# Performance work log

Hardware: AMD Instinct MI355X
Metric: run time of the kernel (lower is better)

Reference implementation:

```python
import jax, jax.numpy as jnp
import numpy as np

HIDDEN = 100   # units per head
HEADS = 8
LAYERS = 3
ALPHA = 0.2    # tf.nn.leaky_relu default


def setup_inputs() -> dict:
    key = jax.random.key(0)
    ks = jax.random.split(key, 10)
    n, feat, E = 50000, 32, 800000
    d = HIDDEN * HEADS  # 800
    scale = 0.05
    node_states = jax.random.normal(ks[0], (n, feat), jnp.float32)
    # TF code's repeat/bincount segment-softmax assumes edges sorted by source
    src = jnp.sort(jax.random.randint(ks[1], (E,), 0, n, dtype=jnp.int32))
    dst = jax.random.randint(ks[2], (E,), 0, n, dtype=jnp.int32)
    W_pre = jax.random.normal(ks[3], (feat, d), jnp.float32) * scale
    b_pre = jnp.zeros((d,), jnp.float32)
    kernels = jax.random.normal(ks[4], (LAYERS, HEADS, d, HIDDEN), jnp.float32) * scale
    att = jax.random.normal(ks[5], (LAYERS, HEADS, 2 * HIDDEN, 1), jnp.float32) * scale
    Wl = jax.random.normal(ks[6], (d, 1), jnp.float32) * scale
    bl = jnp.zeros((1,), jnp.float32)
    Wc = jax.random.normal(ks[7], (n, 1), jnp.float32) * scale
    bc = jnp.zeros((1,), jnp.float32)
    return dict(node_states=node_states, src=src, dst=dst, W_pre=W_pre, b_pre=b_pre,
                kernels=kernels, att=att, Wl=Wl, bl=bl, Wc=Wc, bc=bc)


def _gat_head(x, src, dst, K, A, n):
    # x: (n, d); K: (d, u); A: (2u,) attention vector
    Ht = x @ K                          # (n, u)
    # concat([Ht[src], Ht[dst]]) @ A == Ht[src]@A[:u] + Ht[dst]@A[u:]
    s = Ht @ A[:HIDDEN]                 # (n,)
    t = Ht @ A[HIDDEN:]                 # (n,)
    e = jax.nn.leaky_relu(s[src] + t[dst], ALPHA)   # (E,)
    w = jnp.exp(jnp.clip(e, -2.0, 2.0))             # (E,)
    denom = jax.ops.segment_sum(w, src, num_segments=n)  # (n,)
    wn = w / denom[src]                              # segment softmax, (E,)
    # weighted scatter-add of neighbor features
    return jax.ops.segment_sum(Ht[dst] * wn[:, None], src, num_segments=n)  # (n, u)


def reference(node_states, src, dst, W_pre, b_pre, kernels, att, Wl, bl, Wc, bc):
    n = node_states.shape[0]
    x = jax.nn.relu(node_states @ W_pre + b_pre)     # (n, 800)
    for l in range(LAYERS):
        heads = [_gat_head(x, src, dst, kernels[l, h], att[l, h, :, 0], n)
                 for h in range(HEADS)]
        x = jax.nn.relu(jnp.concatenate(heads, axis=-1)) + x  # residual
    logits = jnp.squeeze(x @ Wl + bl, -1)            # (n,)
    return logits @ Wc + bc                          # critic value, (1,)
```

## Files before the change

### kernel.cpp

```cpp
#include <hip/hip_runtime.h>
#include <math.h>

#define HIDDEN 100
#define HEADS 8
#define D 800
#define ALPHA 0.2f

typedef unsigned short ushort;
typedef unsigned int uint;
typedef __attribute__((ext_vector_type(8))) short bf16x8;
typedef __attribute__((ext_vector_type(4))) float f32x4;

__device__ inline float bf2f(ushort u) { uint x = ((uint)u) << 16; return __uint_as_float(x); }
__device__ inline ushort f2bf(float f) {
    uint u = __float_as_uint(f);
    u += 0x7FFF + ((u >> 16) & 1);
    return (ushort)(u >> 16);
}

__device__ inline void gl_lds16(const void* g, void* l) {
    __builtin_amdgcn_global_load_lds((const __attribute__((address_space(1))) void*)g,
                                     (__attribute__((address_space(3))) void*)l, 16, 0, 0);
}

__global__ void k_rowptr(const int* __restrict__ src, int E, int n, int* __restrict__ row_ptr) {
    int i = blockIdx.x * blockDim.x + threadIdx.x;
    if (i > n) return;
    int lo = 0, hi = E;
    while (lo < hi) { int mid = (lo + hi) >> 1; if (src[mid] < i) lo = mid + 1; else hi = mid; }
    row_ptr[i] = lo;
}

__global__ void k_repack(const float* __restrict__ kin, ushort* __restrict__ bsp) {
    int gid = blockIdx.x * blockDim.x + threadIdx.x;
    if (gid >= 3 * D * D) return;
    int l = gid / (D * D);
    int rem = gid % (D * D);
    int nn = rem / D;
    int k = rem % D;
    int h = nn / HIDDEN, c = nn % HIDDEN;
    float v = kin[((size_t)(l * HEADS + h) * D + k) * HIDDEN + c];
    bsp[((size_t)l * D + nn) * D + k] = f2bf(v);
}

__global__ __launch_bounds__(256) void k_pre(const float* __restrict__ ns, const float* __restrict__ W,
                                             const float* __restrict__ b, ushort* __restrict__ xh,
                                             ushort* __restrict__ xl, int n) {
    int j = blockIdx.x * 256 + threadIdx.x;
    if (j >= D) return;
    float wk[32];
#pragma unroll
    for (int k = 0; k < 32; k++) wk[k] = W[k * D + j];
    float bj = b[j];
    int r0 = blockIdx.y * 32;
    int r1 = min(r0 + 32, n);
    for (int r = r0; r < r1; r++) {
        float acc = bj;
#pragma unroll
        for (int k = 0; k < 32; k++) acc += ns[r * 32 + k] * wk[k];
        acc = fmaxf(acc, 0.f);
        ushort h = f2bf(acc);
        xh[(size_t)r * D + j] = h;
        xl[(size_t)r * D + j] = f2bf(acc - bf2f(h));
    }
}

__global__ __launch_bounds__(256) void k_gemm(const ushort* __restrict__ xh, const ushort* __restrict__ xl,
                                              const ushort* __restrict__ Bsp, ushort* __restrict__ C, int M) {
    __shared__ __align__(16) ushort Af[2][16 * 512];
    __shared__ __align__(16) ushort Bf[2][10 * 512];

    int d = blockIdx.x;
    int q = d & 7, m = d >> 3;
    int c = m % 5, j = m / 5;
    int r = j * 8 + q;
    int nrb = (M + 127) >> 7;
    if (r >= nrb) return;
    int row0 = r * 128, col0 = c * 160;

    int t = threadIdx.x;
    int w = t >> 6, lane = t & 63;
    int wr = w >> 1, wc = w & 1;
    int l15 = lane & 15, ks = lane >> 4;

    const ushort* srcA[4];
    int ldsA[4];
#pragma unroll
    for (int i = 0; i < 4; i++) {
        int g = i * 4 + w;
        int mat = g >> 3, tile = g & 7;
        int row = min(row0 + tile * 16 + l15, M - 1);
        srcA[i] = (mat ? xl : xh) + (size_t)row * D + ks * 8;
        ldsA[i] = g * 512;
    }
    int bcnt = (w < 2) ? 2 : 3;
    int bbase = (w < 2) ? 2 * w : 4 + 3 * (w - 2);
    const ushort* srcB[3];
    int ldsB[3];
#pragma unroll
    for (int i = 0; i < 3; i++) {
        int tile = bbase + i;
        if (tile > 9) tile = 9;
        int col = col0 + tile * 16 + l15;
        srcB[i] = Bsp + (size_t)col * D + ks * 8;
        ldsB[i] = tile * 512;
    }

    f32x4 acc[4][5] = {};

    auto stage = [&](int buf, int k0) {
#pragma unroll
        for (int i = 0; i < 4; i++) gl_lds16(srcA[i] + k0, &Af[buf][ldsA[i]]);
        for (int i = 0; i < bcnt; i++) gl_lds16(srcB[i] + k0, &Bf[buf][ldsB[i]]);
    };
    auto compute = [&](int buf) {
        bf16x8 bh[5];
#pragma unroll
        for (int ni = 0; ni < 5; ni++)
            bh[ni] = *(const bf16x8*)&Bf[buf][(wc * 5 + ni) * 512 + lane * 8];
#pragma unroll
        for (int mi = 0; mi < 4; mi++) {
            int tA = wr * 4 + mi;
            bf16x8 ah = *(const bf16x8*)&Af[buf][tA * 512 + lane * 8];
            bf16x8 al = *(const bf16x8*)&Af[buf][(8 + tA) * 512 + lane * 8];
#pragma unroll
            for (int ni = 0; ni < 5; ni++) {
                acc[mi][ni] = __builtin_amdgcn_mfma_f32_16x16x32_bf16(ah, bh[ni], acc[mi][ni], 0, 0, 0);
                acc[mi][ni] = __builtin_amdgcn_mfma_f32_16x16x32_bf16(al, bh[ni], acc[mi][ni], 0, 0, 0);
            }
        }
    };

    stage(0, 0);
    for (int kt = 0; kt < 25; kt++) {
        if (kt < 24) {
            stage((kt + 1) & 1, (kt + 1) * 32);
            if (w < 2) asm volatile("s_waitcnt vmcnt(6)" ::: "memory");
            else       asm volatile("s_waitcnt vmcnt(7)" ::: "memory");
        } else {
            asm volatile("s_waitcnt vmcnt(0)" ::: "memory");
        }
        __builtin_amdgcn_s_barrier();
        compute(kt & 1);
        __builtin_amdgcn_s_barrier();
    }

#pragma unroll
    for (int mi = 0; mi < 4; mi++) {
#pragma unroll
        for (int ni = 0; ni < 5; ni++) {
            int gr0 = row0 + wr * 64 + mi * 16 + ks * 4;
            int gc = col0 + wc * 80 + ni * 16 + l15;
#pragma unroll
            for (int rr = 0; rr < 4; rr++) {
                int gr = gr0 + rr;
                if (gr < M) C[(size_t)gr * D + gc] = f2bf(acc[mi][ni][rr]);
            }
        }
    }
}

__global__ __launch_bounds__(256) void k_st(const ushort* __restrict__ Ht, const float* __restrict__ att_l,
                                            float* __restrict__ s_all, float* __restrict__ t_all, int n) {
    int gid = blockIdx.x * blockDim.x + threadIdx.x;
    if (gid >= n * HEADS) return;
    int i = gid >> 3, h = gid & 7;
    const uint2* hp2 = (const uint2*)(Ht + (size_t)i * D + h * HIDDEN);
    const float* As = att_l + h * 2 * HIDDEN;
    const float* At = As + HIDDEN;
    float s = 0.f, t = 0.f;
#pragma unroll 5
    for (int q = 0; q < 25; q++) {
        uint2 v = hp2[q];
        float f0 = bf2f((ushort)(v.x & 0xFFFF)), f1 = bf2f((ushort)(v.x >> 16));
        float f2 = bf2f((ushort)(v.y & 0xFFFF)), f3 = bf2f((ushort)(v.y >> 16));
        int c = q * 4;
        s += f0 * As[c] + f1 * As[c + 1] + f2 * As[c + 2] + f3 * As[c + 3];
        t += f0 * At[c] + f1 * At[c + 1] + f2 * At[c + 2] + f3 * At[c + 3];
    }
    s_all[gid] = s;
    t_all[gid] = t;
}

__global__ __launch_bounds__(256) void k_edge(const ushort* __restrict__ Ht, ushort* __restrict__ xh,
                                              ushort* __restrict__ xl,
                                              const float* __restrict__ s_all, const float* __restrict__ t_all,
                                              const int* __restrict__ dst, const int* __restrict__ row_ptr,
                                              int n) {
    int i = blockIdx.x;
    int t = threadIdx.x;
    __shared__ float lw[32][8];
    __shared__ int ld[32];
    int e0 = row_ptr[i], e1 = row_ptr[i + 1];
    int h = t / 25;
    int el = t >> 3, hh = t & 7;
    float s_ih = s_all[i * 8 + hh];
    float acc0 = 0, acc1 = 0, acc2 = 0, acc3 = 0, den = 0;

    for (int base = e0; base < e1; base += 32) {
        int cnt = min(32, e1 - base);
        __syncthreads();
        if (el < cnt) {
            int dd = dst[base + el];
            float ev = s_ih + t_all[dd * 8 + hh];
            ev = ev >= 0.f ? ev : ALPHA * ev;
            ev = fminf(fmaxf(ev, -2.f), 2.f);
            lw[el][hh] = __expf(ev);
            if (hh == 0) ld[el] = dd;
        }
        __syncthreads();
        if (t < 200) {
#pragma unroll 4
            for (int e = 0; e < cnt; e++) {
                int dd = ld[e];
                uint2 v = *(const uint2*)(Ht + (size_t)dd * D + t * 4);
                float wgt = lw[e][h];
                acc0 += wgt * bf2f((ushort)(v.x & 0xFFFF));
                acc1 += wgt * bf2f((ushort)(v.x >> 16));
                acc2 += wgt * bf2f((ushort)(v.y & 0xFFFF));
                acc3 += wgt * bf2f((ushort)(v.y >> 16));
                den += wgt;
            }
        }
    }
    if (t < 200) {
        size_t off = (size_t)i * D + t * 4;
        uint2 vh = *(uint2*)(xh + off);
        uint2 vl = *(uint2*)(xl + off);
        float x0 = bf2f((ushort)(vh.x & 0xFFFF)) + bf2f((ushort)(vl.x & 0xFFFF));
        float x1 = bf2f((ushort)(vh.x >> 16))    + bf2f((ushort)(vl.x >> 16));
        float x2 = bf2f((ushort)(vh.y & 0xFFFF)) + bf2f((ushort)(vl.y & 0xFFFF));
        float x3 = bf2f((ushort)(vh.y >> 16))    + bf2f((ushort)(vl.y >> 16));
        float inv = den > 0.f ? 1.f / den : 0.f;
        x0 += fmaxf(acc0 * inv, 0.f);
        x1 += fmaxf(acc1 * inv, 0.f);
        x2 += fmaxf(acc2 * inv, 0.f);
        x3 += fmaxf(acc3 * inv, 0.f);
        ushort h0 = f2bf(x0), h1 = f2bf(x1), h2 = f2bf(x2), h3 = f2bf(x3);
        ushort l0 = f2bf(x0 - bf2f(h0)), l1 = f2bf(x1 - bf2f(h1));
        ushort l2 = f2bf(x2 - bf2f(h2)), l3 = f2bf(x3 - bf2f(h3));
        *(uint2*)(xh + off) = make_uint2((uint)h0 | ((uint)h1 << 16), (uint)h2 | ((uint)h3 << 16));
        *(uint2*)(xl + off) = make_uint2((uint)l0 | ((uint)l1 << 16), (uint)l2 | ((uint)l3 << 16));
    }
}

__global__ __launch_bounds__(256) void k_final(const ushort* __restrict__ xh, const ushort* __restrict__ xl,
                                               const float* __restrict__ Wl, const float* __restrict__ bl,
                                               const float* __restrict__ Wc, float* __restrict__ fpart, int n) {
    __shared__ float part[4];
    int lane = threadIdx.x & 63, w = threadIdx.x >> 6;
    int wid = blockIdx.x * 4 + w;
    int nw = gridDim.x * 4;
    float p = 0.f;
    for (int i = wid; i < n; i += nw) {
        float dot = 0.f;
#pragma unroll
        for (int r = 0; r < 13; r++) {
            int j = r * 64 + lane;
            if (j < D) {
                size_t off = (size_t)i * D + j;
                dot += (bf2f(xh[off]) + bf2f(xl[off])) * Wl[j];
            }
        }
#pragma unroll
        for (int off = 32; off; off >>= 1) dot += __shfl_xor(dot, off);
        if (lane == 0) p += (dot + bl[0]) * Wc[i];
    }
    if (lane == 0) part[w] = p;
    __syncthreads();
    if (threadIdx.x == 0) fpart[blockIdx.x] = part[0] + part[1] + part[2] + part[3];
}

__global__ __launch_bounds__(64) void k_reduce(const float* __restrict__ fpart, const float* __restrict__ bc,
                                               float* __restrict__ out, int nb) {
    if (threadIdx.x == 0) {
        float s = 0.f;
        for (int q = 0; q < nb; q++) s += fpart[q];
        out[0] = s + bc[0];
    }
}

__global__ void k_sentinel(float* out) { out[0] = 12345.0f; }

extern "C" void kernel_launch(void* const* d_in, const int* in_sizes, int n_in,
                              void* d_out, int out_size, void* d_ws, size_t ws_size,
                              hipStream_t stream) {
    const float* ns   = (const float*)d_in[0];
    const int*   src  = (const int*)d_in[1];
    const int*   dst  = (const int*)d_in[2];
    const float* Wpre = (const float*)d_in[3];
    const float* bpre = (const float*)d_in[4];
    const float* kern = (const float*)d_in[5];
    const float* att  = (const float*)d_in[6];
    const float* Wl   = (const float*)d_in[7];
    const float* bl   = (const float*)d_in[8];
    const float* Wc   = (const float*)d_in[9];
    const float* bc   = (const float*)d_in[10];
    int n = in_sizes[9];
    int E = in_sizes[1];

    size_t need = 0;
    auto sz = [&](size_t bytes) { size_t o = need; need += (bytes + 255) & ~255ull; return o; };
    size_t o_xh    = sz((size_t)n * D * 2);
    size_t o_xl    = sz((size_t)n * D * 2);
    size_t o_Ht    = sz((size_t)n * D * 2);
    size_t o_bsp   = sz(3ull * D * D * 2);
    size_t o_s     = sz((size_t)n * 8 * 4);
    size_t o_t     = sz((size_t)n * 8 * 4);
    size_t o_rp    = sz(((size_t)n + 1) * 4);
    size_t o_fp    = sz(128 * 4);

    if (need > ws_size) {
        k_sentinel<<<1, 1, 0, stream>>>((float*)d_out);
        return;
    }

    char* ws = (char*)d_ws;
    ushort* xh    = (ushort*)(ws + o_xh);
    ushort* xl    = (ushort*)(ws + o_xl);
    ushort* Ht    = (ushort*)(ws + o_Ht);
    ushort* bsp   = (ushort*)(ws + o_bsp);
    float*  s_all = (float*)(ws + o_s);
    float*  t_all = (float*)(ws + o_t);
    int*    row_ptr = (int*)(ws + o_rp);
    float*  fpart = (float*)(ws + o_fp);

    k_rowptr<<<(n + 1 + 255) / 256, 256, 0, stream>>>(src, E, n, row_ptr);
    k_repack<<<(3 * D * D + 255) / 256, 256, 0, stream>>>(kern, bsp);
    dim3 gpre((D + 255) / 256, (n + 31) / 32);
    k_pre<<<gpre, 256, 0, stream>>>(ns, Wpre, bpre, xh, xl, n);

    int nrb = (n + 127) / 128;
    int grid_g = 8 * (((nrb + 7) / 8) * 5);
    for (int l = 0; l < 3; l++) {
        k_gemm<<<grid_g, 256, 0, stream>>>(xh, xl, bsp + (size_t)l * D * D, Ht, n);
        k_st<<<(n * HEADS + 255) / 256, 256, 0, stream>>>(Ht, att + l * HEADS * 2 * HIDDEN, s_all, t_all, n);
        k_edge<<<n, 256, 0, stream>>>(Ht, xh, xl, s_all, t_all, dst, row_ptr, n);
    }

    k_final<<<120, 256, 0, stream>>>(xh, xl, Wl, bl, Wc, fpart, n);
    k_reduce<<<1, 64, 0, stream>>>(fpart, bc, (float*)d_out, 120);
}
```

Measured before the change: 1.432 ms.

## Store Ht head-major and process one head per block in edge gather

The GEMM epilogue now writes Ht in head-major layout [head][node][100], and s/t scores are stored head-major too. The edge kernel now assigns each block one head and 10 source nodes, 25 threads per node. Each thread walks its node's edges directly and recomputes the attention weight itself, with no shared-memory staging or barriers. The aim is to keep each head's 10 MB slice of Ht hot in L2 while gathering, and to drop synchronisation. In exchange, dst and t are read redundantly, 6 of 256 threads sit idle, and GEMM stores become strided.

Measured after the change: 1.575 ms. 1.1x slower.

```diff
diff --git a/kernel.cpp b/kernel.cpp
--- a/kernel.cpp
+++ b/kernel.cpp
@@ -146,15 +146,17 @@
     }
 
 #pragma unroll
-    for (int mi = 0; mi < 4; mi++) {
-#pragma unroll
-        for (int ni = 0; ni < 5; ni++) {
+    for (int ni = 0; ni < 5; ni++) {
+        int gc = col0 + wc * 80 + ni * 16 + l15;
+        int hd = gc / 100, cc = gc - hd * 100;
+        size_t hbase = (size_t)hd * M * 100 + cc;
+#pragma unroll
+        for (int mi = 0; mi < 4; mi++) {
             int gr0 = row0 + wr * 64 + mi * 16 + ks * 4;
-            int gc = col0 + wc * 80 + ni * 16 + l15;
 #pragma unroll
             for (int rr = 0; rr < 4; rr++) {
                 int gr = gr0 + rr;
-                if (gr < M) C[(size_t)gr * D + gc] = f2bf(acc[mi][ni][rr]);
+                if (gr < M) C[hbase + (size_t)gr * 100] = f2bf(acc[mi][ni][rr]);
             }
         }
     }
@@ -165,7 +167,7 @@
     int gid = blockIdx.x * blockDim.x + threadIdx.x;
     if (gid >= n * HEADS) return;
     int i = gid >> 3, h = gid & 7;
-    const uint2* hp2 = (const uint2*)(Ht + (size_t)i * D + h * HIDDEN);
+    const uint2* hp2 = (const uint2*)(Ht + ((size_t)h * n + i) * HIDDEN);
     const float* As = att_l + h * 2 * HIDDEN;
     const float* At = As + HIDDEN;
     float s = 0.f, t = 0.f;
@@ -178,8 +180,8 @@
         s += f0 * As[c] + f1 * As[c + 1] + f2 * As[c + 2] + f3 * As[c + 3];
         t += f0 * At[c] + f1 * At[c + 1] + f2 * At[c + 2] + f3 * At[c + 3];
     }
-    s_all[gid] = s;
-    t_all[gid] = t;
+    s_all[(size_t)h * n + i] = s;
+    t_all[(size_t)h * n + i] = t;
 }
 
 __global__ __launch_bounds__(256) void k_edge(const ushort* __restrict__ Ht, ushort* __restrict__ xh,
@@ -187,61 +189,52 @@
                                               const float* __restrict__ s_all, const float* __restrict__ t_all,
                                               const int* __restrict__ dst, const int* __restrict__ row_ptr,
                                               int n) {
-    int i = blockIdx.x;
+    int d = blockIdx.x;
+    int h = d & 7, g = d >> 3;
     int t = threadIdx.x;
-    __shared__ float lw[32][8];
-    __shared__ int ld[32];
+    int sub = t / 25, c = t - sub * 25;
+    if (sub >= 10) return;
+    int i = g * 10 + sub;
+    if (i >= n) return;
+
     int e0 = row_ptr[i], e1 = row_ptr[i + 1];
-    int h = t / 25;
-    int el = t >> 3, hh = t & 7;
-    float s_ih = s_all[i * 8 + hh];
-    float acc0 = 0, acc1 = 0, acc2 = 0, acc3 = 0, den = 0;
-
-    for (int base = e0; base < e1; base += 32) {
-        int cnt = min(32, e1 - base);
-        __syncthreads();
-        if (el < cnt) {
-            int dd = dst[base + el];
-            float ev = s_ih + t_all[dd * 8 + hh];
-            ev = ev >= 0.f ? ev : ALPHA * ev;
-            ev = fminf(fmaxf(ev, -2.f), 2.f);
-            lw[el][hh] = __expf(ev);
-            if (hh == 0) ld[el] = dd;
-        }
-        __syncthreads();
-        if (t < 200) {
-#pragma unroll 4
-            for (int e = 0; e < cnt; e++) {
-                int dd = ld[e];
-                uint2 v = *(const uint2*)(Ht + (size_t)dd * D + t * 4);
-                float wgt = lw[e][h];
-                acc0 += wgt * bf2f((ushort)(v.x & 0xFFFF));
-                acc1 += wgt * bf2f((ushort)(v.x >> 16));
-                acc2 += wgt * bf2f((ushort)(v.y & 0xFFFF));
-                acc3 += wgt * bf2f((ushort)(v.y >> 16));
-                den += wgt;
-            }
-        }
-    }
-    if (t < 200) {
-        size_t off = (size_t)i * D + t * 4;
-        uint2 vh = *(uint2*)(xh + off);
-        uint2 vl = *(uint2*)(xl + off);
-        float x0 = bf2f((ushort)(vh.x & 0xFFFF)) + bf2f((ushort)(vl.x & 0xFFFF));
-        float x1 = bf2f((ushort)(vh.x >> 16))    + bf2f((ushort)(vl.x >> 16));
-        float x2 = bf2f((ushort)(vh.y & 0xFFFF)) + bf2f((ushort)(vl.y & 0xFFFF));
-        float x3 = bf2f((ushort)(vh.y >> 16))    + bf2f((ushort)(vl.y >> 16));
-        float inv = den > 0.f ? 1.f / den : 0.f;
-        x0 += fmaxf(acc0 * inv, 0.f);
-        x1 += fmaxf(acc1 * inv, 0.f);
-        x2 += fmaxf(acc2 * inv, 0.f);
-        x3 += fmaxf(acc3 * inv, 0.f);
-        ushort h0 = f2bf(x0), h1 = f2bf(x1), h2 = f2bf(x2), h3 = f2bf(x3);
-        ushort l0 = f2bf(x0 - bf2f(h0)), l1 = f2bf(x1 - bf2f(h1));
-        ushort l2 = f2bf(x2 - bf2f(h2)), l3 = f2bf(x3 - bf2f(h3));
-        *(uint2*)(xh + off) = make_uint2((uint)h0 | ((uint)h1 << 16), (uint)h2 | ((uint)h3 << 16));
-        *(uint2*)(xl + off) = make_uint2((uint)l0 | ((uint)l1 << 16), (uint)l2 | ((uint)l3 << 16));
-    }
+    float s_ih = s_all[(size_t)h * n + i];
+    const float* t_h = t_all + (size_t)h * n;
+    const ushort* Ht_h = Ht + (size_t)h * n * HIDDEN;
+
+    float a0 = 0, a1 = 0, a2 = 0, a3 = 0, den = 0;
+#pragma unroll 2
+    for (int e = e0; e < e1; e++) {
+        int dd = dst[e];
+        float ev = s_ih + t_h[dd];
+        ev = ev >= 0.f ? ev : ALPHA * ev;
+        ev = fminf(fmaxf(ev, -2.f), 2.f);
+        float wgt = __expf(ev);
+        uint2 v = *(const uint2*)(Ht_h + (size_t)dd * HIDDEN + c * 4);
+        a0 += wgt * bf2f((ushort)(v.x & 0xFFFF));
+        a1 += wgt * bf2f((ushort)(v.x >> 16));
+        a2 += wgt * bf2f((ushort)(v.y & 0xFFFF));
+        a3 += wgt * bf2f((ushort)(v.y >> 16));
+        den += wgt;
+    }
+
+    size_t off = (size_t)i * D + h * HIDDEN + c * 4;
+    uint2 vh = *(uint2*)(xh + off);
+    uint2 vl = *(uint2*)(xl + off);
+    float x0 = bf2f((ushort)(vh.x & 0xFFFF)) + bf2f((ushort)(vl.x & 0xFFFF));
+    float x1 = bf2f((ushort)(vh.x >> 16))    + bf2f((ushort)(vl.x >> 16));
+    float x2 = bf2f((ushort)(vh.y & 0xFFFF)) + bf2f((ushort)(vl.y & 0xFFFF));
+    float x3 = bf2f((ushort)(vh.y >> 16))    + bf2f((ushort)(vl.y >> 16));
+    float inv = den > 0.f ? 1.f / den : 0.f;
+    x0 += fmaxf(a0 * inv, 0.f);
+    x1 += fmaxf(a1 * inv, 0.f);
+    x2 += fmaxf(a2 * inv, 0.f);
+    x3 += fmaxf(a3 * inv, 0.f);
+    ushort h0 = f2bf(x0), h1 = f2bf(x1), h2 = f2bf(x2), h3 = f2bf(x3);
+    ushort l0 = f2bf(x0 - bf2f(h0)), l1 = f2bf(x1 - bf2f(h1));
+    ushort l2 = f2bf(x2 - bf2f(h2)), l3 = f2bf(x3 - bf2f(h3));
+    *(uint2*)(xh + off) = make_uint2((uint)h0 | ((uint)h1 << 16), (uint)h2 | ((uint)h3 << 16));
+    *(uint2*)(xl + off) = make_uint2((uint)l0 | ((uint)l1 << 16), (uint)l2 | ((uint)l3 << 16));
 }
 
 __global__ __launch_bounds__(256) void k_final(const ushort* __restrict__ xh, const ushort* __restrict__ xl,
@@ -332,10 +325,11 @@
 
     int nrb = (n + 127) / 128;
     int grid_g = 8 * (((nrb + 7) / 8) * 5);
+    int grid_e = 8 * ((n + 9) / 10);
     for (int l = 0; l < 3; l++) {
         k_gemm<<<grid_g, 256, 0, stream>>>(xh, xl, bsp + (size_t)l * D * D, Ht, n);
         k_st<<<(n * HEADS + 255) / 256, 256, 0, stream>>>(Ht, att + l * HEADS * 2 * HIDDEN, s_all, t_all, n);
-        k_edge<<<n, 256, 0, stream>>>(Ht, xh, xl, s_all, t_all, dst, row_ptr, n);
+        k_edge<<<grid_e, 256, 0, stream>>>(Ht, xh, xl, s_all, t_all, dst, row_ptr, n);
     }
 
     k_final<<<120, 256, 0, stream>>>(xh, xl, Wl, bl, Wc, fpart, n);
```
